# Kernel tuning notes

Hardware: AMD Instinct MI355X
Metric: run time of the kernel (lower is better)

The kernel has to match this reference:

```python
import jax, jax.numpy as jnp
import numpy as np

T = 8  # number of DP iterations (self.T)

def setup_inputs() -> dict:
    key = jax.random.key(0)
    ks = jax.random.split(key, 9)
    bs, dims, L, d = 16, 4, 2048, 256
    x = jax.random.uniform(ks[0], (bs, dims, L), dtype=jnp.float32)  # one-hot-like input
    s_in = 1.0 / np.sqrt(dims)
    s_d = 1.0 / np.sqrt(d)
    W1 = jax.random.uniform(ks[1], (d, dims), minval=-s_in, maxval=s_in, dtype=jnp.float32)
    b1 = jax.random.uniform(ks[2], (d,), minval=-s_in, maxval=s_in, dtype=jnp.float32)
    W2 = jax.random.uniform(ks[3], (d, d), minval=-s_d, maxval=s_d, dtype=jnp.float32)
    b2 = jax.random.uniform(ks[4], (d,), minval=-s_d, maxval=s_d, dtype=jnp.float32)
    W3 = jax.random.uniform(ks[5], (d, dims), minval=-s_in, maxval=s_in, dtype=jnp.float32)
    b3 = jax.random.uniform(ks[6], (d,), minval=-s_in, maxval=s_in, dtype=jnp.float32)
    W4 = jax.random.uniform(ks[7], (d, d), minval=-s_d, maxval=s_d, dtype=jnp.float32)
    b4 = jax.random.uniform(ks[8], (d,), minval=-s_d, maxval=s_d, dtype=jnp.float32)
    return dict(x=x, W1=W1, b1=b1, W2=W2, b2=b2, W3=W3, b3=b3, W4=W4, b4=b4)

def reference(x, W1, b1, W2, b2, W3, b3, W4, b4):
    # x: (bs, dims, L). The original allocates V:(bs,T+1,L+2,L+2,d) but only the
    # two diagonals V[i,j,j+1] ("up") and V[i,j,j-1] ("down") are ever written/read,
    # so the recurrence collapses to two (bs,L,d) lanes.
    a = jnp.einsum('bdl,od->blo', x, W1) + b1  # W1(x_j) for all j: (bs, L, d)
    bs, L, d = a.shape
    zcol = jnp.zeros((bs, 1, d), a.dtype)
    shift_r = lambda v: jnp.concatenate([zcol, v[:, :-1]], axis=1)  # v[j-1], zero at j=0
    shift_l = lambda v: jnp.concatenate([v[:, 1:], zcol], axis=1)   # v[j+1], zero at j=L-1
    up = jnp.zeros_like(a)   # up[j]   = V[i, j+1, j+2] (0-indexed lane)
    down = jnp.zeros_like(a) # down[j] = V[i, j+1, j]
    for _ in range(T):
        up = jax.nn.relu(a + shift_r(up) @ W2.T + b2)
        down = jax.nn.relu(a + shift_l(down) @ W2.T + b2)
    c = jnp.einsum('bdl,od->blo', x, W3) + b3
    # miu[j] = relu(W3 x_j + W4(V[T,j-1,j]) + W4(V[T,j+1,j]))
    miu = jax.nn.relu(c + (shift_r(up) @ W4.T + b4) + (shift_l(down) @ W4.T + b4))
    return miu  # (bs, L, d)
```

## Files before the change

### kernel.cpp

```cpp
#include <hip/hip_runtime.h>


typedef __bf16 bf16x8 __attribute__((ext_vector_type(8)));
typedef __bf16 bf16x4 __attribute__((ext_vector_type(4)));
typedef float f32x16 __attribute__((ext_vector_type(16)));
typedef unsigned int uint2v __attribute__((ext_vector_type(2)));

#define MFMA32(a, b, c) __builtin_amdgcn_mfma_f32_32x32x16_bf16(a, b, c, 0, 0, 0)

__device__ __forceinline__ unsigned short f2bf(float f) {
  unsigned int u = __builtin_bit_cast(unsigned int, f);
  u += 0x7fffu + ((u >> 16) & 1u);
  return (unsigned short)(u >> 16);
}

__global__ void prep_kernel(const float* __restrict__ W1, const float* __restrict__ b1,
                            const float* __restrict__ W2, const float* __restrict__ b2,
                            const float* __restrict__ W3, const float* __restrict__ b3,
                            const float* __restrict__ W4, const float* __restrict__ b4,
                            unsigned short* __restrict__ ws) {
  int idx = blockIdx.x * 256 + threadIdx.x;
  if (idx >= 139264) return;
  float v = 0.0f;
  if (idx < 131072) {
    const float* W = (idx < 65536) ? W2 : W4;
    int i = idx & 65535;
    int j = i & 7, f = i >> 3;
    int lane = f & 63, slot = f >> 6;
    int ks = slot & 15, ot = slot >> 4;
    int o = ot * 32 + (lane & 31);
    int k = ks * 16 + (lane >> 5) * 8 + j;
    v = W[o * 256 + k];
  } else {
    int i = idx - 131072;
    bool first = (i < 4096);
    int ii = i & 4095;
    int j = ii & 7, f = ii >> 3;
    int lane = f & 63, ot = f >> 6;
    int o = ot * 32 + (lane & 31);
    if (lane < 32) {
      if (j < 4) v = first ? W1[o * 4 + j] : W3[o * 4 + j];
      else if (j == 4) v = first ? (b1[o] + b2[o]) : (b3[o] + 2.0f * b4[o]);
    }
  }
  ws[idx] = f2bf(v);
}

#define NC 14

__global__ __launch_bounds__(256, 2)
void chain_kernel(const float* __restrict__ x, const unsigned short* __restrict__ ws,
                  float* __restrict__ out) {
  __shared__ int4 U[2][32 * 64];
  __shared__ int4 xw[80];
  __shared__ int4 zc;

  const int tid = threadIdx.x;
  const int l = tid & 63;
  const int w = tid >> 6;
  const int lane31 = l & 31;
  const int khalf = l >> 5;
  const int tile = blockIdx.x;
  const int b = tile >> 5;
  const int j0 = (tile & 31) * 64;

  const int4* w2f = (const int4*)ws;
  const int4* w4f = (const int4*)(ws + 65536);
  const int4* w1xg = (const int4*)(ws + 131072);
  const int4* w3xg = (const int4*)(ws + 135168);

  if (tid == 0) zc = make_int4(0, 0, 0, 0);
  if (tid < 80) {
    int j = j0 - 8 + tid;
    int4 c = make_int4(0, 0, 0, 0);
    if (j >= 0 && j < 2048) {
      const float* xb = x + (b * 4) * 2048 + j;
      unsigned short h0 = f2bf(xb[0]);
      unsigned short h1 = f2bf(xb[2048]);
      unsigned short h2 = f2bf(xb[4096]);
      unsigned short h3 = f2bf(xb[6144]);
      c = make_int4((int)(h0 | ((unsigned int)h1 << 16)),
                    (int)(h2 | ((unsigned int)h3 << 16)),
                    0x00003f80, 0);
    }
    xw[tid] = c;
  }

  const int ot0 = w * 2;
  bf16x8 w2c[2][NC];
  bf16x8 w1x[2];
#pragma unroll
  for (int t2 = 0; t2 < 2; ++t2) {
    w1x[t2] = __builtin_bit_cast(bf16x8, w1xg[(ot0 + t2) * 64 + l]);
#pragma unroll
    for (int ks = 0; ks < NC; ++ks)
      w2c[t2][ks] = __builtin_bit_cast(bf16x8, w2f[((ot0 + t2) * 16 + ks) * 64 + l]);
  }
  __syncthreads();

  const int mrow0 = lane31;
  const int mrow1 = 32 + lane31;

  int4 zk[2][2][2];

#pragma unroll 1
  for (int half = 0; half < 16; ++half) {
    const int t = (half >> 1) + 1;
    const int ph = half & 1;

    bf16x8 afs[2][2];
#pragma unroll
    for (int s = 0; s < 2; ++s) {
      afs[s][0] = __builtin_bit_cast(bf16x8, w2f[(ot0 * 16 + NC + s) * 64 + l]);
      afs[s][1] = __builtin_bit_cast(bf16x8, w2f[((ot0 + 1) * 16 + NC + s) * 64 + l]);
    }

    f32x16 acc[2][2] = {};

    if (half > 0) {
      int4* Uw = U[ph ^ 1];
#pragma unroll
      for (int mt = 0; mt < 2; ++mt)
#pragma unroll
        for (int t2 = 0; t2 < 2; ++t2)
#pragma unroll
          for (int p = 0; p < 2; ++p)
            Uw[((ot0 + t2) * 4 + 2 * p + khalf) * 64 + mt * 32 + lane31] = zk[mt][t2][p];
    }

    __builtin_amdgcn_s_setprio(1);

#pragma unroll
    for (int mt = 0; mt < 2; ++mt) {
      int m = mt ? mrow1 : mrow0;
      int widx = (ph == 0) ? (m + t - 1) : (m + 17 - t);
      const int4* p = (l < 32) ? (xw + widx) : (&zc);
      bf16x8 bx = __builtin_bit_cast(bf16x8, *p);
      acc[mt][0] = MFMA32(w1x[0], bx, acc[mt][0]);
      acc[mt][1] = MFMA32(w1x[1], bx, acc[mt][1]);
    }

    if (t > 1) {
      const int4* Ur = U[ph];
#pragma unroll
      for (int ks = 0; ks < 16; ++ks) {
        int c0 = 2 * ks + khalf;
        bf16x8 bu0 = __builtin_bit_cast(bf16x8, Ur[c0 * 64 + mrow0]);
        bf16x8 bu1 = __builtin_bit_cast(bf16x8, Ur[c0 * 64 + mrow1]);
        bf16x8 af0, af1;
        if (ks < NC) { af0 = w2c[0][ks]; af1 = w2c[1][ks]; }
        else         { af0 = afs[ks - NC][0]; af1 = afs[ks - NC][1]; }
        acc[0][0] = MFMA32(af0, bu0, acc[0][0]);
        acc[0][1] = MFMA32(af1, bu0, acc[0][1]);
        acc[1][0] = MFMA32(af0, bu1, acc[1][0]);
        acc[1][1] = MFMA32(af1, bu1, acc[1][1]);
      }
    }

    __builtin_amdgcn_s_setprio(0);

#pragma unroll
    for (int mt = 0; mt < 2; ++mt) {
#pragma unroll
      for (int t2 = 0; t2 < 2; ++t2) {
        unsigned lo[4], hi[4];
#pragma unroll
        for (int q = 0; q < 4; ++q) {
          bf16x4 h;
          h.x = (__bf16)fmaxf(acc[mt][t2][4 * q + 0], 0.0f);
          h.y = (__bf16)fmaxf(acc[mt][t2][4 * q + 1], 0.0f);
          h.z = (__bf16)fmaxf(acc[mt][t2][4 * q + 2], 0.0f);
          h.w = (__bf16)fmaxf(acc[mt][t2][4 * q + 3], 0.0f);
          uint2 u = __builtin_bit_cast(uint2, h);
          lo[q] = u.x; hi[q] = u.y;
        }
        uint2v r0 = __builtin_amdgcn_permlane32_swap(lo[0], lo[1], false, false);
        uint2v r1 = __builtin_amdgcn_permlane32_swap(hi[0], hi[1], false, false);
        zk[mt][t2][0] = make_int4((int)r0.x, (int)r1.x, (int)r0.y, (int)r1.y);
        uint2v r2 = __builtin_amdgcn_permlane32_swap(lo[2], lo[3], false, false);
        uint2v r3 = __builtin_amdgcn_permlane32_swap(hi[2], hi[3], false, false);
        zk[mt][t2][1] = make_int4((int)r2.x, (int)r3.x, (int)r2.y, (int)r3.y);
      }
    }
    __syncthreads();
  }

  {
    int4* Uw = U[1];
#pragma unroll
    for (int mt = 0; mt < 2; ++mt)
#pragma unroll
      for (int t2 = 0; t2 < 2; ++t2)
#pragma unroll
        for (int p = 0; p < 2; ++p)
          Uw[((ot0 + t2) * 4 + 2 * p + khalf) * 64 + mt * 32 + lane31] = zk[mt][t2][p];
  }
  __syncthreads();

  {
    f32x16 acc[2][2] = {};
    bf16x8 w3x0 = __builtin_bit_cast(bf16x8, w3xg[ot0 * 64 + l]);
    bf16x8 w3x1 = __builtin_bit_cast(bf16x8, w3xg[(ot0 + 1) * 64 + l]);
    __builtin_amdgcn_s_setprio(1);
#pragma unroll
    for (int mt = 0; mt < 2; ++mt) {
      int m = mt ? mrow1 : mrow0;
      const int4* p = (l < 32) ? (xw + m + 8) : (&zc);
      bf16x8 bx = __builtin_bit_cast(bf16x8, *p);
      acc[mt][0] = MFMA32(w3x0, bx, acc[mt][0]);
      acc[mt][1] = MFMA32(w3x1, bx, acc[mt][1]);
    }
#pragma unroll 1
    for (int ph = 0; ph < 2; ++ph) {
      const int4* Sp = U[ph];
#pragma unroll
      for (int ks = 0; ks < 16; ++ks) {
        int c0 = 2 * ks + khalf;
        bf16x8 bu0 = __builtin_bit_cast(bf16x8, Sp[c0 * 64 + mrow0]);
        bf16x8 bu1 = __builtin_bit_cast(bf16x8, Sp[c0 * 64 + mrow1]);
        bf16x8 af0 = __builtin_bit_cast(bf16x8, w4f[(ot0 * 16 + ks) * 64 + l]);
        bf16x8 af1 = __builtin_bit_cast(bf16x8, w4f[((ot0 + 1) * 16 + ks) * 64 + l]);
        acc[0][0] = MFMA32(af0, bu0, acc[0][0]);
        acc[0][1] = MFMA32(af1, bu0, acc[0][1]);
        acc[1][0] = MFMA32(af0, bu1, acc[1][0]);
        acc[1][1] = MFMA32(af1, bu1, acc[1][1]);
      }
    }
    __builtin_amdgcn_s_setprio(0);
#pragma unroll
    for (int mt = 0; mt < 2; ++mt) {
      int m = mt ? mrow1 : mrow0;
      int pbase = (b * 2048 + j0 + m) * 256;
#pragma unroll
      for (int t2 = 0; t2 < 2; ++t2) {
#pragma unroll
        for (int q = 0; q < 4; ++q) {
          int ob = (ot0 + t2) * 32 + 8 * q + 4 * khalf;
          float4 v;
          v.x = fmaxf(acc[mt][t2][4 * q + 0], 0.0f);
          v.y = fmaxf(acc[mt][t2][4 * q + 1], 0.0f);
          v.z = fmaxf(acc[mt][t2][4 * q + 2], 0.0f);
          v.w = fmaxf(acc[mt][t2][4 * q + 3], 0.0f);
          *(float4*)(out + pbase + ob) = v;
        }
      }
    }
  }
}

extern "C" void kernel_launch(void* const* d_in, const int* in_sizes, int n_in,
                              void* d_out, int out_size, void* d_ws, size_t ws_size,
                              hipStream_t stream) {
  const float* x  = (const float*)d_in[0];
  const float* W1 = (const float*)d_in[1];
  const float* b1 = (const float*)d_in[2];
  const float* W2 = (const float*)d_in[3];
  const float* b2 = (const float*)d_in[4];
  const float* W3 = (const float*)d_in[5];
  const float* b3 = (const float*)d_in[6];
  const float* W4 = (const float*)d_in[7];
  const float* b4 = (const float*)d_in[8];
  unsigned short* ws = (unsigned short*)d_ws;

  prep_kernel<<<544, 256, 0, stream>>>(W1, b1, W2, b2, W3, b3, W4, b4, ws);
  chain_kernel<<<512, 256, 0, stream>>>(x, ws, (float*)d_out);
}
```

Baseline: 131.2 us.

## Feed each warp's own output chunk from registers and rotate K order per warp

Each wave now starts its K loop at its own output slice (4*w) and takes those four K-chunks straight from the packed registers it just produced, so fewer LDS reads are needed. The up and down lanes are kept in two register sets with an unrolled pair of intervals, which removes the runtime phase branching. NC drops from 14 to 10, and the leftover W2 fragments are prefetched in stages inside the loop. The final W4 pass also reads its own slice from registers. The aims are less LDS read traffic and fewer bank conflicts, traded against more global/L2 weight reloads per interval and higher register pressure.

Result: slower. 177.0 us (+34.9%).

```diff
diff --git a/kernel.cpp b/kernel.cpp
--- a/kernel.cpp
+++ b/kernel.cpp
@@ -46,7 +46,113 @@
   ws[idx] = f2bf(v);
 }
 
-#define NC 14
+#define NC 10
+
+#define LOAD_AFS2(S0) { \
+    int ksr_ = (4 * w + NC + (S0)) & 15; \
+    afs[S0][0] = __builtin_bit_cast(bf16x8, w2f[(ot0 * 16 + ksr_) * 64 + l]); \
+    afs[S0][1] = __builtin_bit_cast(bf16x8, w2f[((ot0 + 1) * 16 + ksr_) * 64 + l]); \
+    ksr_ = (4 * w + NC + (S0) + 1) & 15; \
+    afs[(S0) + 1][0] = __builtin_bit_cast(bf16x8, w2f[(ot0 * 16 + ksr_) * 64 + l]); \
+    afs[(S0) + 1][1] = __builtin_bit_cast(bf16x8, w2f[((ot0 + 1) * 16 + ksr_) * 64 + l]); }
+
+#define PACK(ZS) \
+  _Pragma("unroll") for (int mt = 0; mt < 2; ++mt) { \
+    _Pragma("unroll") for (int t2 = 0; t2 < 2; ++t2) { \
+      unsigned lo[4], hi[4]; \
+      _Pragma("unroll") for (int q = 0; q < 4; ++q) { \
+        bf16x4 h; \
+        h.x = (__bf16)fmaxf(acc[mt][t2][4 * q + 0], 0.0f); \
+        h.y = (__bf16)fmaxf(acc[mt][t2][4 * q + 1], 0.0f); \
+        h.z = (__bf16)fmaxf(acc[mt][t2][4 * q + 2], 0.0f); \
+        h.w = (__bf16)fmaxf(acc[mt][t2][4 * q + 3], 0.0f); \
+        uint2 u = __builtin_bit_cast(uint2, h); \
+        lo[q] = u.x; hi[q] = u.y; \
+      } \
+      uint2v r0 = __builtin_amdgcn_permlane32_swap(lo[0], lo[1], false, false); \
+      uint2v r1 = __builtin_amdgcn_permlane32_swap(hi[0], hi[1], false, false); \
+      ZS[mt][t2][0] = make_int4((int)r0.x, (int)r1.x, (int)r0.y, (int)r1.y); \
+      uint2v r2 = __builtin_amdgcn_permlane32_swap(lo[2], lo[3], false, false); \
+      uint2v r3 = __builtin_amdgcn_permlane32_swap(hi[2], hi[3], false, false); \
+      ZS[mt][t2][1] = make_int4((int)r2.x, (int)r3.x, (int)r2.y, (int)r3.y); \
+    } \
+  }
+
+#define INTERVAL(PH, T, ZS, ZO, DOW, DOG) { \
+  bf16x8 afs[16 - NC][2]; \
+  if (DOG) LOAD_AFS2(0) \
+  f32x16 acc[2][2] = {}; \
+  if (DOW) { \
+    int4* Uw = U[(PH) ^ 1]; \
+    _Pragma("unroll") for (int mt = 0; mt < 2; ++mt) \
+    _Pragma("unroll") for (int t2 = 0; t2 < 2; ++t2) \
+    _Pragma("unroll") for (int p = 0; p < 2; ++p) \
+      Uw[((ot0 + t2) * 4 + 2 * p + khalf) * 64 + mt * 32 + lane31] = ZO[mt][t2][p]; \
+  } \
+  __builtin_amdgcn_s_setprio(1); \
+  _Pragma("unroll") for (int mt = 0; mt < 2; ++mt) { \
+    int m = mt ? mrow1 : mrow0; \
+    int widx = (PH) == 0 ? (m + (T) - 1) : (m + 17 - (T)); \
+    const int4* p = (l < 32) ? (xw + widx) : (&zc); \
+    bf16x8 bx = __builtin_bit_cast(bf16x8, *p); \
+    acc[mt][0] = MFMA32(w1x[0], bx, acc[mt][0]); \
+    acc[mt][1] = MFMA32(w1x[1], bx, acc[mt][1]); \
+  } \
+  if (DOG) { \
+    _Pragma("unroll") for (int s = 0; s < 4; ++s) { \
+      bf16x8 bu0 = __builtin_bit_cast(bf16x8, ZS[0][s >> 1][s & 1]); \
+      bf16x8 bu1 = __builtin_bit_cast(bf16x8, ZS[1][s >> 1][s & 1]); \
+      acc[0][0] = MFMA32(w2c[0][s], bu0, acc[0][0]); \
+      acc[0][1] = MFMA32(w2c[1][s], bu0, acc[0][1]); \
+      acc[1][0] = MFMA32(w2c[0][s], bu1, acc[1][0]); \
+      acc[1][1] = MFMA32(w2c[1][s], bu1, acc[1][1]); \
+    } \
+    LOAD_AFS2(2) \
+    const int4* Ur = U[PH]; \
+    _Pragma("unroll") for (int i = 4; i < 16; ++i) { \
+      if (i == 8) LOAD_AFS2(4) \
+      int ksr = (4 * w + i) & 15; \
+      int c0 = 2 * ksr + khalf; \
+      bf16x8 bu0 = __builtin_bit_cast(bf16x8, Ur[c0 * 64 + mrow0]); \
+      bf16x8 bu1 = __builtin_bit_cast(bf16x8, Ur[c0 * 64 + mrow1]); \
+      bf16x8 af0 = (i < NC) ? w2c[0][i] : afs[i - NC][0]; \
+      bf16x8 af1 = (i < NC) ? w2c[1][i] : afs[i - NC][1]; \
+      acc[0][0] = MFMA32(af0, bu0, acc[0][0]); \
+      acc[0][1] = MFMA32(af1, bu0, acc[0][1]); \
+      acc[1][0] = MFMA32(af0, bu1, acc[1][0]); \
+      acc[1][1] = MFMA32(af1, bu1, acc[1][1]); \
+    } \
+  } \
+  __builtin_amdgcn_s_setprio(0); \
+  PACK(ZS) \
+  __syncthreads(); \
+}
+
+#define FINAL_PH(PH, ZS) { \
+  const int4* Sp = U[PH]; \
+  _Pragma("unroll") for (int s = 0; s < 4; ++s) { \
+    int ksr = 4 * w + s; \
+    bf16x8 af0 = __builtin_bit_cast(bf16x8, w4f[(ot0 * 16 + ksr) * 64 + l]); \
+    bf16x8 af1 = __builtin_bit_cast(bf16x8, w4f[((ot0 + 1) * 16 + ksr) * 64 + l]); \
+    bf16x8 bu0 = __builtin_bit_cast(bf16x8, ZS[0][s >> 1][s & 1]); \
+    bf16x8 bu1 = __builtin_bit_cast(bf16x8, ZS[1][s >> 1][s & 1]); \
+    acc[0][0] = MFMA32(af0, bu0, acc[0][0]); \
+    acc[0][1] = MFMA32(af1, bu0, acc[0][1]); \
+    acc[1][0] = MFMA32(af0, bu1, acc[1][0]); \
+    acc[1][1] = MFMA32(af1, bu1, acc[1][1]); \
+  } \
+  _Pragma("unroll") for (int i = 4; i < 16; ++i) { \
+    int ksr = (4 * w + i) & 15; \
+    int c0 = 2 * ksr + khalf; \
+    bf16x8 bu0 = __builtin_bit_cast(bf16x8, Sp[c0 * 64 + mrow0]); \
+    bf16x8 bu1 = __builtin_bit_cast(bf16x8, Sp[c0 * 64 + mrow1]); \
+    bf16x8 af0 = __builtin_bit_cast(bf16x8, w4f[(ot0 * 16 + ksr) * 64 + l]); \
+    bf16x8 af1 = __builtin_bit_cast(bf16x8, w4f[((ot0 + 1) * 16 + ksr) * 64 + l]); \
+    acc[0][0] = MFMA32(af0, bu0, acc[0][0]); \
+    acc[0][1] = MFMA32(af1, bu0, acc[0][1]); \
+    acc[1][0] = MFMA32(af0, bu1, acc[1][0]); \
+    acc[1][1] = MFMA32(af1, bu1, acc[1][1]); \
+  } }
 
 __global__ __launch_bounds__(256, 2)
 void chain_kernel(const float* __restrict__ x, const unsigned short* __restrict__ ws,
@@ -93,96 +199,25 @@
   for (int t2 = 0; t2 < 2; ++t2) {
     w1x[t2] = __builtin_bit_cast(bf16x8, w1xg[(ot0 + t2) * 64 + l]);
 #pragma unroll
-    for (int ks = 0; ks < NC; ++ks)
-      w2c[t2][ks] = __builtin_bit_cast(bf16x8, w2f[((ot0 + t2) * 16 + ks) * 64 + l]);
+    for (int i = 0; i < NC; ++i) {
+      int ksr = (4 * w + i) & 15;
+      w2c[t2][i] = __builtin_bit_cast(bf16x8, w2f[((ot0 + t2) * 16 + ksr) * 64 + l]);
+    }
   }
   __syncthreads();
 
   const int mrow0 = lane31;
   const int mrow1 = 32 + lane31;
 
-  int4 zk[2][2][2];
+  int4 zkU[2][2][2], zkD[2][2][2];
+
+  INTERVAL(0, 1, zkU, zkD, false, false)
+  INTERVAL(1, 1, zkD, zkU, true, false)
 
 #pragma unroll 1
-  for (int half = 0; half < 16; ++half) {
-    const int t = (half >> 1) + 1;
-    const int ph = half & 1;
-
-    bf16x8 afs[2][2];
-#pragma unroll
-    for (int s = 0; s < 2; ++s) {
-      afs[s][0] = __builtin_bit_cast(bf16x8, w2f[(ot0 * 16 + NC + s) * 64 + l]);
-      afs[s][1] = __builtin_bit_cast(bf16x8, w2f[((ot0 + 1) * 16 + NC + s) * 64 + l]);
-    }
-
-    f32x16 acc[2][2] = {};
-
-    if (half > 0) {
-      int4* Uw = U[ph ^ 1];
-#pragma unroll
-      for (int mt = 0; mt < 2; ++mt)
-#pragma unroll
-        for (int t2 = 0; t2 < 2; ++t2)
-#pragma unroll
-          for (int p = 0; p < 2; ++p)
-            Uw[((ot0 + t2) * 4 + 2 * p + khalf) * 64 + mt * 32 + lane31] = zk[mt][t2][p];
-    }
-
-    __builtin_amdgcn_s_setprio(1);
-
-#pragma unroll
-    for (int mt = 0; mt < 2; ++mt) {
-      int m = mt ? mrow1 : mrow0;
-      int widx = (ph == 0) ? (m + t - 1) : (m + 17 - t);
-      const int4* p = (l < 32) ? (xw + widx) : (&zc);
-      bf16x8 bx = __builtin_bit_cast(bf16x8, *p);
-      acc[mt][0] = MFMA32(w1x[0], bx, acc[mt][0]);
-      acc[mt][1] = MFMA32(w1x[1], bx, acc[mt][1]);
-    }
-
-    if (t > 1) {
-      const int4* Ur = U[ph];
-#pragma unroll
-      for (int ks = 0; ks < 16; ++ks) {
-        int c0 = 2 * ks + khalf;
-        bf16x8 bu0 = __builtin_bit_cast(bf16x8, Ur[c0 * 64 + mrow0]);
-        bf16x8 bu1 = __builtin_bit_cast(bf16x8, Ur[c0 * 64 + mrow1]);
-        bf16x8 af0, af1;
-        if (ks < NC) { af0 = w2c[0][ks]; af1 = w2c[1][ks]; }
-        else         { af0 = afs[ks - NC][0]; af1 = afs[ks - NC][1]; }
-        acc[0][0] = MFMA32(af0, bu0, acc[0][0]);
-        acc[0][1] = MFMA32(af1, bu0, acc[0][1]);
-        acc[1][0] = MFMA32(af0, bu1, acc[1][0]);
-        acc[1][1] = MFMA32(af1, bu1, acc[1][1]);
-      }
-    }
-
-    __builtin_amdgcn_s_setprio(0);
-
-#pragma unroll
-    for (int mt = 0; mt < 2; ++mt) {
-#pragma unroll
-      for (int t2 = 0; t2 < 2; ++t2) {
-        unsigned lo[4], hi[4];
-#pragma unroll
-        for (int q = 0; q < 4; ++q) {
-          bf16x4 h;
-          h.x = (__bf16)fmaxf(acc[mt][t2][4 * q + 0], 0.0f);
-          h.y = (__bf16)fmaxf(acc[mt][t2][4 * q + 1], 0.0f);
-          h.z = (__bf16)fmaxf(acc[mt][t2][4 * q + 2], 0.0f);
-          h.w = (__bf16)fmaxf(acc[mt][t2][4 * q + 3], 0.0f);
-          uint2 u = __builtin_bit_cast(uint2, h);
-          lo[q] = u.x; hi[q] = u.y;
-        }
-        uint2v r0 = __builtin_amdgcn_permlane32_swap(lo[0], lo[1], false, false);
-        uint2v r1 = __builtin_amdgcn_permlane32_swap(hi[0], hi[1], false, false);
-        zk[mt][t2][0] = make_int4((int)r0.x, (int)r1.x, (int)r0.y, (int)r1.y);
-        uint2v r2 = __builtin_amdgcn_permlane32_swap(lo[2], lo[3], false, false);
-        uint2v r3 = __builtin_amdgcn_permlane32_swap(hi[2], hi[3], false, false);
-        zk[mt][t2][1] = make_int4((int)r2.x, (int)r3.x, (int)r2.y, (int)r3.y);
-      }
-    }
-    __syncthreads();
+  for (int tt = 1; tt < 8; ++tt) {
+    INTERVAL(0, tt + 1, zkU, zkD, true, true)
+    INTERVAL(1, tt + 1, zkD, zkU, true, true)
   }
 
   {
@@ -193,7 +228,7 @@
       for (int t2 = 0; t2 < 2; ++t2)
 #pragma unroll
         for (int p = 0; p < 2; ++p)
-          Uw[((ot0 + t2) * 4 + 2 * p + khalf) * 64 + mt * 32 + lane31] = zk[mt][t2][p];
+          Uw[((ot0 + t2) * 4 + 2 * p + khalf) * 64 + mt * 32 + lane31] = zkD[mt][t2][p];
   }
   __syncthreads();
 
@@ -210,22 +245,8 @@
       acc[mt][0] = MFMA32(w3x0, bx, acc[mt][0]);
       acc[mt][1] = MFMA32(w3x1, bx, acc[mt][1]);
     }
-#pragma unroll 1
-    for (int ph = 0; ph < 2; ++ph) {
-      const int4* Sp = U[ph];
-#pragma unroll
-      for (int ks = 0; ks < 16; ++ks) {
-        int c0 = 2 * ks + khalf;
-        bf16x8 bu0 = __builtin_bit_cast(bf16x8, Sp[c0 * 64 + mrow0]);
-        bf16x8 bu1 = __builtin_bit_cast(bf16x8, Sp[c0 * 64 + mrow1]);
-        bf16x8 af0 = __builtin_bit_cast(bf16x8, w4f[(ot0 * 16 + ks) * 64 + l]);
-        bf16x8 af1 = __builtin_bit_cast(bf16x8, w4f[((ot0 + 1) * 16 + ks) * 64 + l]);
-        acc[0][0] = MFMA32(af0, bu0, acc[0][0]);
-        acc[0][1] = MFMA32(af1, bu0, acc[0][1]);
-        acc[1][0] = MFMA32(af0, bu1, acc[1][0]);
-        acc[1][1] = MFMA32(af1, bu1, acc[1][1]);
-      }
-    }
+    FINAL_PH(0, zkU)
+    FINAL_PH(1, zkD)
     __builtin_amdgcn_s_setprio(0);
 #pragma unroll
     for (int mt = 0; mt < 2; ++mt) {
```

## Halve tile width to 32 rows, double grid, interleave up/down chains per step

Applied to the files above, without the earlier changes.

Each block now handles 32 positions instead of 64, so the grid doubles to 1024 blocks and each warp keeps all 16 W2 k-slices in registers instead of reloading two from global every step. The up and down recurrences are processed back to back within one iteration with separate double-buffered LDS lanes, giving one barrier per time step instead of two. Results are written straight to LDS instead of being held in registers across the barrier. The trade-off is half the MFMA work per block per step, so there are more blocks that each need their own weight register load, and halo reuse per block drops.

Result: slower. 134.7 us (+2.7%).

```diff
diff --git a/kernel.cpp b/kernel.cpp
--- a/kernel.cpp
+++ b/kernel.cpp
@@ -46,13 +46,56 @@
   ws[idx] = f2bf(v);
 }
 
-#define NC 14
+#define GSTEP(RB, KS) { \
+    bf16x8 bu_ = __builtin_bit_cast(bf16x8, (RB)[(2 * (KS) + khalf) * 32 + lane31]); \
+    acc[0] = MFMA32(w2c[0][KS], bu_, acc[0]); \
+    acc[1] = MFMA32(w2c[1][KS], bu_, acc[1]); }
+
+#define PACKWRITE(WB) { \
+    _Pragma("unroll") for (int t2 = 0; t2 < 2; ++t2) { \
+      unsigned lo[4], hi[4]; \
+      _Pragma("unroll") for (int q = 0; q < 4; ++q) { \
+        bf16x4 h; \
+        h.x = (__bf16)fmaxf(acc[t2][4 * q + 0], 0.0f); \
+        h.y = (__bf16)fmaxf(acc[t2][4 * q + 1], 0.0f); \
+        h.z = (__bf16)fmaxf(acc[t2][4 * q + 2], 0.0f); \
+        h.w = (__bf16)fmaxf(acc[t2][4 * q + 3], 0.0f); \
+        uint2 u = __builtin_bit_cast(uint2, h); \
+        lo[q] = u.x; hi[q] = u.y; \
+      } \
+      uint2v r0 = __builtin_amdgcn_permlane32_swap(lo[0], lo[1], false, false); \
+      uint2v r1 = __builtin_amdgcn_permlane32_swap(hi[0], hi[1], false, false); \
+      (WB)[((ot0 + t2) * 4 + khalf) * 32 + lane31] = \
+          make_int4((int)r0.x, (int)r1.x, (int)r0.y, (int)r1.y); \
+      uint2v r2 = __builtin_amdgcn_permlane32_swap(lo[2], lo[3], false, false); \
+      uint2v r3 = __builtin_amdgcn_permlane32_swap(hi[2], hi[3], false, false); \
+      (WB)[((ot0 + t2) * 4 + 2 + khalf) * 32 + lane31] = \
+          make_int4((int)r2.x, (int)r3.x, (int)r2.y, (int)r3.y); \
+    } }
+
+#define INTERVAL(PH, T, RB, WB, DOG) { \
+  f32x16 acc[2] = {}; \
+  { int widx = (PH) == 0 ? (lane31 + (T) - 1) : (lane31 + 17 - (T)); \
+    const int4* p_ = (l < 32) ? (xw + widx) : (&zc); \
+    bf16x8 bx_ = __builtin_bit_cast(bf16x8, *p_); \
+    acc[0] = MFMA32(w1x[0], bx_, acc[0]); \
+    acc[1] = MFMA32(w1x[1], bx_, acc[1]); } \
+  if (DOG) { \
+    __builtin_amdgcn_s_setprio(1); \
+    GSTEP(RB, 0)  GSTEP(RB, 1)  GSTEP(RB, 2)  GSTEP(RB, 3) \
+    GSTEP(RB, 4)  GSTEP(RB, 5)  GSTEP(RB, 6)  GSTEP(RB, 7) \
+    GSTEP(RB, 8)  GSTEP(RB, 9)  GSTEP(RB, 10) GSTEP(RB, 11) \
+    GSTEP(RB, 12) GSTEP(RB, 13) GSTEP(RB, 14) GSTEP(RB, 15) \
+    __builtin_amdgcn_s_setprio(0); \
+  } \
+  PACKWRITE(WB) }
 
 __global__ __launch_bounds__(256, 2)
 void chain_kernel(const float* __restrict__ x, const unsigned short* __restrict__ ws,
                   float* __restrict__ out) {
-  __shared__ int4 U[2][32 * 64];
-  __shared__ int4 xw[80];
+  __shared__ int4 UA[2][1024];
+  __shared__ int4 UB[2][1024];
+  __shared__ int4 xw[48];
   __shared__ int4 zc;
 
   const int tid = threadIdx.x;
@@ -61,8 +104,8 @@
   const int lane31 = l & 31;
   const int khalf = l >> 5;
   const int tile = blockIdx.x;
-  const int b = tile >> 5;
-  const int j0 = (tile & 31) * 64;
+  const int b = tile >> 6;
+  const int j0 = (tile & 63) * 32;
 
   const int4* w2f = (const int4*)ws;
   const int4* w4f = (const int4*)(ws + 65536);
@@ -70,7 +113,7 @@
   const int4* w3xg = (const int4*)(ws + 135168);
 
   if (tid == 0) zc = make_int4(0, 0, 0, 0);
-  if (tid < 80) {
+  if (tid < 48) {
     int j = j0 - 8 + tid;
     int4 c = make_int4(0, 0, 0, 0);
     if (j >= 0 && j < 2048) {
@@ -87,162 +130,68 @@
   }
 
   const int ot0 = w * 2;
-  bf16x8 w2c[2][NC];
+  bf16x8 w2c[2][16];
   bf16x8 w1x[2];
 #pragma unroll
   for (int t2 = 0; t2 < 2; ++t2) {
     w1x[t2] = __builtin_bit_cast(bf16x8, w1xg[(ot0 + t2) * 64 + l]);
 #pragma unroll
-    for (int ks = 0; ks < NC; ++ks)
-      w2c[t2][ks] = __builtin_bit_cast(bf16x8, w2f[((ot0 + t2) * 16 + ks) * 64 + l]);
+    for (int i = 0; i < 16; ++i)
+      w2c[t2][i] = __builtin_bit_cast(bf16x8, w2f[((ot0 + t2) * 16 + i) * 64 + l]);
   }
   __syncthreads();
 
-  const int mrow0 = lane31;
-  const int mrow1 = 32 + lane31;
-
-  int4 zk[2][2][2];
+  INTERVAL(0, 1, UA[0], UA[0], false)
+  INTERVAL(1, 1, UB[0], UB[0], false)
+  __syncthreads();
 
 #pragma unroll 1
-  for (int half = 0; half < 16; ++half) {
-    const int t = (half >> 1) + 1;
-    const int ph = half & 1;
-
-    bf16x8 afs[2][2];
-#pragma unroll
-    for (int s = 0; s < 2; ++s) {
-      afs[s][0] = __builtin_bit_cast(bf16x8, w2f[(ot0 * 16 + NC + s) * 64 + l]);
-      afs[s][1] = __builtin_bit_cast(bf16x8, w2f[((ot0 + 1) * 16 + NC + s) * 64 + l]);
-    }
-
-    f32x16 acc[2][2] = {};
-
-    if (half > 0) {
-      int4* Uw = U[ph ^ 1];
-#pragma unroll
-      for (int mt = 0; mt < 2; ++mt)
-#pragma unroll
-        for (int t2 = 0; t2 < 2; ++t2)
-#pragma unroll
-          for (int p = 0; p < 2; ++p)
-            Uw[((ot0 + t2) * 4 + 2 * p + khalf) * 64 + mt * 32 + lane31] = zk[mt][t2][p];
-    }
-
+  for (int k = 1; k < 8; ++k) {
+    const int4* ra = UA[(k - 1) & 1];
+    int4* wa = UA[k & 1];
+    const int4* rb = UB[(k - 1) & 1];
+    int4* wb = UB[k & 1];
+    const int T = k + 1;
+    INTERVAL(0, T, ra, wa, true)
+    INTERVAL(1, T, rb, wb, true)
+    __syncthreads();
+  }
+
+  {
+    f32x16 acc[2] = {};
+    { int widx = lane31 + 8;
+      const int4* p_ = (l < 32) ? (xw + widx) : (&zc);
+      bf16x8 bx = __builtin_bit_cast(bf16x8, *p_);
+      bf16x8 w3x0 = __builtin_bit_cast(bf16x8, w3xg[ot0 * 64 + l]);
+      bf16x8 w3x1 = __builtin_bit_cast(bf16x8, w3xg[(ot0 + 1) * 64 + l]);
+      acc[0] = MFMA32(w3x0, bx, acc[0]);
+      acc[1] = MFMA32(w3x1, bx, acc[1]); }
     __builtin_amdgcn_s_setprio(1);
-
-#pragma unroll
-    for (int mt = 0; mt < 2; ++mt) {
-      int m = mt ? mrow1 : mrow0;
-      int widx = (ph == 0) ? (m + t - 1) : (m + 17 - t);
-      const int4* p = (l < 32) ? (xw + widx) : (&zc);
-      bf16x8 bx = __builtin_bit_cast(bf16x8, *p);
-      acc[mt][0] = MFMA32(w1x[0], bx, acc[mt][0]);
-      acc[mt][1] = MFMA32(w1x[1], bx, acc[mt][1]);
-    }
-
-    if (t > 1) {
-      const int4* Ur = U[ph];
-#pragma unroll
-      for (int ks = 0; ks < 16; ++ks) {
-        int c0 = 2 * ks + khalf;
-        bf16x8 bu0 = __builtin_bit_cast(bf16x8, Ur[c0 * 64 + mrow0]);
-        bf16x8 bu1 = __builtin_bit_cast(bf16x8, Ur[c0 * 64 + mrow1]);
-        bf16x8 af0, af1;
-        if (ks < NC) { af0 = w2c[0][ks]; af1 = w2c[1][ks]; }
-        else         { af0 = afs[ks - NC][0]; af1 = afs[ks - NC][1]; }
-        acc[0][0] = MFMA32(af0, bu0, acc[0][0]);
-        acc[0][1] = MFMA32(af1, bu0, acc[0][1]);
-        acc[1][0] = MFMA32(af0, bu1, acc[1][0]);
-        acc[1][1] = MFMA32(af1, bu1, acc[1][1]);
-      }
-    }
-
-    __builtin_amdgcn_s_setprio(0);
-
-#pragma unroll
-    for (int mt = 0; mt < 2; ++mt) {
-#pragma unroll
-      for (int t2 = 0; t2 < 2; ++t2) {
-        unsigned lo[4], hi[4];
-#pragma unroll
-        for (int q = 0; q < 4; ++q) {
-          bf16x4 h;
-          h.x = (__bf16)fmaxf(acc[mt][t2][4 * q + 0], 0.0f);
-          h.y = (__bf16)fmaxf(acc[mt][t2][4 * q + 1], 0.0f);
-          h.z = (__bf16)fmaxf(acc[mt][t2][4 * q + 2], 0.0f);
-          h.w = (__bf16)fmaxf(acc[mt][t2][4 * q + 3], 0.0f);
-          uint2 u = __builtin_bit_cast(uint2, h);
-          lo[q] = u.x; hi[q] = u.y;
-        }
-        uint2v r0 = __builtin_amdgcn_permlane32_swap(lo[0], lo[1], false, false);
-        uint2v r1 = __builtin_amdgcn_permlane32_swap(hi[0], hi[1], false, false);
-        zk[mt][t2][0] = make_int4((int)r0.x, (int)r1.x, (int)r0.y, (int)r1.y);
-        uint2v r2 = __builtin_amdgcn_permlane32_swap(lo[2], lo[3], false, false);
-        uint2v r3 = __builtin_amdgcn_permlane32_swap(hi[2], hi[3], false, false);
-        zk[mt][t2][1] = make_int4((int)r2.x, (int)r3.x, (int)r2.y, (int)r3.y);
-      }
-    }
-    __syncthreads();
-  }
-
-  {
-    int4* Uw = U[1];
-#pragma unroll
-    for (int mt = 0; mt < 2; ++mt)
-#pragma unroll
-      for (int t2 = 0; t2 < 2; ++t2)
-#pragma unroll
-        for (int p = 0; p < 2; ++p)
-          Uw[((ot0 + t2) * 4 + 2 * p + khalf) * 64 + mt * 32 + lane31] = zk[mt][t2][p];
-  }
-  __syncthreads();
-
-  {
-    f32x16 acc[2][2] = {};
-    bf16x8 w3x0 = __builtin_bit_cast(bf16x8, w3xg[ot0 * 64 + l]);
-    bf16x8 w3x1 = __builtin_bit_cast(bf16x8, w3xg[(ot0 + 1) * 64 + l]);
-    __builtin_amdgcn_s_setprio(1);
-#pragma unroll
-    for (int mt = 0; mt < 2; ++mt) {
-      int m = mt ? mrow1 : mrow0;
-      const int4* p = (l < 32) ? (xw + m + 8) : (&zc);
-      bf16x8 bx = __builtin_bit_cast(bf16x8, *p);
-      acc[mt][0] = MFMA32(w3x0, bx, acc[mt][0]);
-      acc[mt][1] = MFMA32(w3x1, bx, acc[mt][1]);
-    }
 #pragma unroll 1
     for (int ph = 0; ph < 2; ++ph) {
-      const int4* Sp = U[ph];
+      const int4* Sp = ph ? UB[1] : UA[1];
 #pragma unroll
       for (int ks = 0; ks < 16; ++ks) {
-        int c0 = 2 * ks + khalf;
-        bf16x8 bu0 = __builtin_bit_cast(bf16x8, Sp[c0 * 64 + mrow0]);
-        bf16x8 bu1 = __builtin_bit_cast(bf16x8, Sp[c0 * 64 + mrow1]);
         bf16x8 af0 = __builtin_bit_cast(bf16x8, w4f[(ot0 * 16 + ks) * 64 + l]);
         bf16x8 af1 = __builtin_bit_cast(bf16x8, w4f[((ot0 + 1) * 16 + ks) * 64 + l]);
-        acc[0][0] = MFMA32(af0, bu0, acc[0][0]);
-        acc[0][1] = MFMA32(af1, bu0, acc[0][1]);
-        acc[1][0] = MFMA32(af0, bu1, acc[1][0]);
-        acc[1][1] = MFMA32(af1, bu1, acc[1][1]);
+        bf16x8 bu = __builtin_bit_cast(bf16x8, Sp[(2 * ks + khalf) * 32 + lane31]);
+        acc[0] = MFMA32(af0, bu, acc[0]);
+        acc[1] = MFMA32(af1, bu, acc[1]);
       }
     }
     __builtin_amdgcn_s_setprio(0);
-#pragma unroll
-    for (int mt = 0; mt < 2; ++mt) {
-      int m = mt ? mrow1 : mrow0;
-      int pbase = (b * 2048 + j0 + m) * 256;
-#pragma unroll
-      for (int t2 = 0; t2 < 2; ++t2) {
-#pragma unroll
-        for (int q = 0; q < 4; ++q) {
-          int ob = (ot0 + t2) * 32 + 8 * q + 4 * khalf;
-          float4 v;
-          v.x = fmaxf(acc[mt][t2][4 * q + 0], 0.0f);
-          v.y = fmaxf(acc[mt][t2][4 * q + 1], 0.0f);
-          v.z = fmaxf(acc[mt][t2][4 * q + 2], 0.0f);
-          v.w = fmaxf(acc[mt][t2][4 * q + 3], 0.0f);
-          *(float4*)(out + pbase + ob) = v;
-        }
+    int pbase = (b * 2048 + j0 + lane31) * 256;
+#pragma unroll
+    for (int t2 = 0; t2 < 2; ++t2) {
+#pragma unroll
+      for (int q = 0; q < 4; ++q) {
+        int ob = (ot0 + t2) * 32 + 8 * q + 4 * khalf;
+        float4 v;
+        v.x = fmaxf(acc[t2][4 * q + 0], 0.0f);
+        v.y = fmaxf(acc[t2][4 * q + 1], 0.0f);
+        v.z = fmaxf(acc[t2][4 * q + 2], 0.0f);
+        v.w = fmaxf(acc[t2][4 * q + 3], 0.0f);
+        *(float4*)(out + pbase + ob) = v;
       }
     }
   }
@@ -263,5 +212,5 @@
   unsigned short* ws = (unsigned short*)d_ws;
 
   prep_kernel<<<544, 256, 0, stream>>>(W1, b1, W2, b2, W3, b3, W4, b4, ws);
-  chain_kernel<<<512, 256, 0, stream>>>(x, ws, (float*)d_out);
-}
+  chain_kernel<<<1024, 256, 0, stream>>>(x, ws, (float*)d_out);
+}
```
